# Kernel tuning notes

Measured on AMD Instinct MI355X. Metric: run time of the kernel, lower is better.

Reference implementation:

```python
import jax, jax.numpy as jnp
import numpy as np

DIM = 1024
HEADS = 16
DIM_HEAD = 64
SCALE = DIM_HEAD ** -0.5
LN_EPS = 1e-5


def layer_norm(x, g, b):
    mu = jnp.mean(x, axis=-1, keepdims=True)
    var = jnp.mean(jnp.square(x - mu), axis=-1, keepdims=True)
    return (x - mu) * jax.lax.rsqrt(var + LN_EPS) * g + b


def setup_inputs() -> dict:
    key = jax.random.key(0)
    ks = jax.random.split(key, 8)
    w_std = DIM ** -0.5  # keep GEMM outputs O(1)
    return {
        "query": jax.random.normal(ks[0], (4, 512, DIM), jnp.float32),
        "kv": jax.random.normal(ks[1], (4, 2048, DIM), jnp.float32),
        "ln_q_g": jnp.ones((DIM,), jnp.float32),
        "ln_q_b": jnp.zeros((DIM,), jnp.float32),
        "ln_kv_g": jnp.ones((DIM,), jnp.float32),
        "ln_kv_b": jnp.zeros((DIM,), jnp.float32),
        "Wq": jax.random.normal(ks[2], (DIM, DIM), jnp.float32) * w_std,
        "bq": jnp.zeros((DIM,), jnp.float32),
        "Wk": jax.random.normal(ks[3], (DIM, DIM), jnp.float32) * w_std,
        "bk": jnp.zeros((DIM,), jnp.float32),
        "Wv": jax.random.normal(ks[4], (DIM, DIM), jnp.float32) * w_std,
        "bv": jnp.zeros((DIM,), jnp.float32),
        "Wo": jax.random.normal(ks[5], (DIM, DIM), jnp.float32) * w_std,
        "bo": jnp.zeros((DIM,), jnp.float32),
    }


def reference(query, kv, ln_q_g, ln_q_b, ln_kv_g, ln_kv_b,
              Wq, bq, Wk, bk, Wv, bv, Wo, bo):
    kv_n = layer_norm(kv, ln_kv_g, ln_kv_b)            # (b, n_kv, d)
    residual = query
    q_n = layer_norm(query, ln_q_g, ln_q_b)            # (b, n_q, d)

    q = q_n @ Wq + bq                                   # (b, n_q, inner)
    kv_input = jnp.concatenate((kv_n, q_n), axis=-2)    # (b, n_kv+n_q, d)
    k = kv_input @ Wk + bk
    v = kv_input @ Wv + bv

    def split_heads(t):
        b, n, _ = t.shape
        return t.reshape(b, n, HEADS, DIM_HEAD).transpose(0, 2, 1, 3)  # b h n dh

    q = split_heads(q) * SCALE
    k = split_heads(k)
    v = split_heads(v)

    sim = jnp.einsum('bhid,bhjd->bhij', q, k)           # (b, h, n_q, n_kv+n_q)
    sim = sim - jax.lax.stop_gradient(jnp.max(sim, axis=-1, keepdims=True))
    attn = jax.nn.softmax(sim, axis=-1)
    out = jnp.einsum('bhij,bhjd->bhid', attn, v)        # (b, h, n_q, dh)

    b, h, n, dh = out.shape
    out = out.transpose(0, 2, 1, 3).reshape(b, n, h * dh)
    return out @ Wo + bo + residual
```

## Files before the change

kernel.cpp:

```cpp
#include <hip/hip_runtime.h>
#include <hip/hip_bf16.h>

#define B_    4
#define NQ    512
#define NKV   2048
#define NT    2560
#define DIM_  1024
#define HEADS 16
#define DH    64
#define NSEQT 10240
#define SCALE_Q_L2E 0.18033688011112042f

typedef short bf16x8 __attribute__((ext_vector_type(8)));
typedef float f32x4  __attribute__((ext_vector_type(4)));
typedef __hip_bfloat16 bf16;

__device__ inline void gll16(const bf16* g, bf16* l) {
  __builtin_amdgcn_global_load_lds(
      (const __attribute__((address_space(1))) unsigned int*)g,
      (__attribute__((address_space(3))) unsigned int*)l, 16, 0, 0);
}

__global__ __launch_bounds__(256) void ln_kernel(
    const float* __restrict__ query, const float* __restrict__ kv,
    const float* __restrict__ gq, const float* __restrict__ bq,
    const float* __restrict__ gkv, const float* __restrict__ bkv,
    bf16* __restrict__ X)
{
  int row = blockIdx.x;
  int b = row / NT, r = row % NT;
  const float *src, *g, *bb;
  if (r < NKV) { src = kv    + ((size_t)b*NKV + r)*DIM_;        g = gkv; bb = bkv; }
  else         { src = query + ((size_t)b*NQ + (r-NKV))*DIM_;   g = gq;  bb = bq;  }
  int t = threadIdx.x;
  float4 v = ((const float4*)src)[t];
  float s  = v.x+v.y+v.z+v.w;
  float s2 = v.x*v.x+v.y*v.y+v.z*v.z+v.w*v.w;
  #pragma unroll
  for (int m=1;m<64;m<<=1){ s += __shfl_xor(s,m,64); s2 += __shfl_xor(s2,m,64); }
  __shared__ float sh[8];
  int wave=t>>6, lane=t&63;
  if(lane==0){ sh[wave]=s; sh[4+wave]=s2; }
  __syncthreads();
  s  = sh[0]+sh[1]+sh[2]+sh[3];
  s2 = sh[4]+sh[5]+sh[6]+sh[7];
  float mu = s*(1.0f/DIM_);
  float rs = rsqrtf(s2*(1.0f/DIM_) - mu*mu + 1e-5f);
  float4 gg = ((const float4*)g)[t];
  float4 b4 = ((const float4*)bb)[t];
  bf16* dst = X + (size_t)row*DIM_ + t*4;
  dst[0]=__float2bfloat16((v.x-mu)*rs*gg.x + b4.x);
  dst[1]=__float2bfloat16((v.y-mu)*rs*gg.y + b4.y);
  dst[2]=__float2bfloat16((v.z-mu)*rs*gg.z + b4.z);
  dst[3]=__float2bfloat16((v.w-mu)*rs*gg.w + b4.w);
}

__global__ __launch_bounds__(256) void trw4_kernel(
    const float* __restrict__ W0, const float* __restrict__ W1,
    const float* __restrict__ W2, const float* __restrict__ W3,
    bf16* __restrict__ T0, bf16* __restrict__ T1,
    bf16* __restrict__ T2, bf16* __restrict__ T3)
{
  const float* W; bf16* Wt;
  switch (blockIdx.z) {
    case 0: W=W0; Wt=T0; break;
    case 1: W=W1; Wt=T1; break;
    case 2: W=W2; Wt=T2; break;
    default: W=W3; Wt=T3; break;
  }
  __shared__ __align__(16) bf16 Ws[64*72];
  int t = threadIdx.x;
  int k0 = blockIdx.x*64, n0 = blockIdx.y*64;
  int kr = t>>2, nseg = (t&3)*16;
  const float4* s4 = (const float4*)(W + (size_t)(k0+kr)*DIM_ + n0 + nseg);
  union { uint4 u[2]; bf16 h[16]; } pk;
  #pragma unroll
  for (int j=0;j<4;j++){
    float4 v = s4[j];
    pk.h[j*4+0]=__float2bfloat16(v.x); pk.h[j*4+1]=__float2bfloat16(v.y);
    pk.h[j*4+2]=__float2bfloat16(v.z); pk.h[j*4+3]=__float2bfloat16(v.w);
  }
  *(uint4*)(Ws + kr*72 + nseg)     = pk.u[0];
  *(uint4*)(Ws + kr*72 + nseg + 8) = pk.u[1];
  __syncthreads();
  int n = t&63, kseg = t>>6;
  union { uint4 u[2]; bf16 h[16]; } o;
  #pragma unroll
  for (int k=0;k<16;k++) o.h[k] = Ws[(kseg*16+k)*72 + n];
  bf16* dst = Wt + (size_t)(n0+n)*DIM_ + k0 + kseg*16;
  *(uint4*)dst = o.u[0];
  *(uint4*)(dst+8) = o.u[1];
}

template<int MODE>
__global__ __launch_bounds__(256) void gemm128(
    const bf16* __restrict__ A, const bf16* __restrict__ Wt,
    const float* __restrict__ bias, const float* __restrict__ residual,
    void* __restrict__ outv, int rows_per_batch, int row_offset,
    int a_batch_stride_rows, int n_seq, float scale)
{
  __shared__ __align__(16) bf16 As[128*32];
  __shared__ __align__(16) bf16 Bs[128*32];
  const int t = threadIdx.x;
  const int m0 = blockIdx.x*128, n0 = blockIdx.y*128;
  const int r0 = t>>2, c8 = (t&3)*8;

  int gm0 = m0 + r0, gm1 = m0 + 64 + r0;
  int b0i = gm0 / rows_per_batch, b1i = gm1 / rows_per_batch;
  const bf16* a0 = A + ((size_t)b0i*a_batch_stride_rows + row_offset + (gm0 - b0i*rows_per_batch))*DIM_ + c8;
  const bf16* a1 = A + ((size_t)b1i*a_batch_stride_rows + row_offset + (gm1 - b1i*rows_per_batch))*DIM_ + c8;
  const bf16* wb0 = Wt + (size_t)(n0 + r0)*DIM_ + c8;
  const bf16* wb1 = Wt + (size_t)(n0 + 64 + r0)*DIM_ + c8;
  bf16* lA0 = As + t*8;  bf16* lA1 = As + 64*32 + t*8;
  bf16* lB0 = Bs + t*8;  bf16* lB1 = Bs + 64*32 + t*8;

  const int wave = t>>6, lane = t&63, qq = lane>>4, mr = lane&15;
  const int wm = (wave>>1)*64, wn = (wave&1)*64;

  f32x4 acc[4][4] = {};
  for (int k0 = 0; k0 < DIM_; k0 += 32) {
    gll16(a0 + k0, lA0);
    gll16(a1 + k0, lA1);
    gll16(wb0 + k0, lB0);
    gll16(wb1 + k0, lB1);
    __syncthreads();
    bf16x8 af[4], bfr[4];
    #pragma unroll
    for (int ms=0;ms<4;ms++) af[ms]  = *(const bf16x8*)(As + (wm+ms*16+mr)*32 + qq*8);
    #pragma unroll
    for (int ns=0;ns<4;ns++) bfr[ns] = *(const bf16x8*)(Bs + (wn+ns*16+mr)*32 + qq*8);
    #pragma unroll
    for (int ms=0;ms<4;ms++)
      #pragma unroll
      for (int ns=0;ns<4;ns++)
        acc[ms][ns] = __builtin_amdgcn_mfma_f32_16x16x32_bf16(af[ms], bfr[ns], acc[ms][ns], 0,0,0);
    __syncthreads();
  }

  if (MODE == 0) {
    float* out = (float*)outv;
    #pragma unroll
    for (int ms=0;ms<4;ms++) {
      int row = m0 + wm + ms*16 + qq*4;
      #pragma unroll
      for (int ns=0;ns<4;ns++) {
        int col = n0 + wn + ns*16 + mr;
        float bc = bias[col];
        #pragma unroll
        for (int r=0;r<4;r++) {
          size_t idx = (size_t)(row+r)*DIM_ + col;
          out[idx] = acc[ms][ns][r] + bc + residual[idx];
        }
      }
    }
  } else if (MODE == 1) {
    bf16* out = (bf16*)outv;
    #pragma unroll
    for (int ms=0;ms<4;ms++) {
      int gmb = m0 + wm + ms*16 + qq*4;
      size_t rowbase[4];
      #pragma unroll
      for (int r=0;r<4;r++) {
        int gm = gmb + r;
        int bb = gm / rows_per_batch;
        int n  = gm - bb*rows_per_batch;
        rowbase[r] = ((size_t)bb*HEADS*n_seq + n)*DH;
      }
      #pragma unroll
      for (int ns=0;ns<4;ns++) {
        int col = n0 + wn + ns*16 + mr;
        int hh = col>>6, dh = col&63;
        float bc = bias[col];
        size_t hoff = (size_t)hh*n_seq*DH + dh;
        #pragma unroll
        for (int r=0;r<4;r++)
          out[rowbase[r] + hoff] = __float2bfloat16((acc[ms][ns][r] + bc)*scale);
      }
    }
  } else {
    bf16* out = (bf16*)outv;
    #pragma unroll
    for (int ms=0;ms<4;ms++) {
      int ch = m0 + wm + ms*16 + qq*4;
      #pragma unroll
      for (int r=0;r<4;r++) {
        float bc = bias[ch+r];
        #pragma unroll
        for (int ns=0;ns<4;ns++) {
          int col = n0 + wn + ns*16 + mr;
          out[(size_t)(ch+r)*NSEQT + col] = __float2bfloat16(acc[ms][ns][r] + bc);
        }
      }
    }
  }
}

__global__ __launch_bounds__(256) void attn5_kernel(
    const bf16* __restrict__ Qh, const bf16* __restrict__ Kh,
    const bf16* __restrict__ VTg, bf16* __restrict__ Ctx)
{
  __shared__ __align__(16) bf16 KV[2][8192];
  __shared__ __align__(16) unsigned int Ps[4][576];

  const int t = threadIdx.x, wave = t>>6, lane = t&63;
  const int qq = lane>>4, mr = lane&15;
  const int blk = blockIdx.x;
  const int bh = (blk&7)*8 + (blk>>6);
  const int q0 = ((blk>>3)&7)*64;
  const int b = bh>>4, h = bh&15;

  const int sl = t>>2, sc = t&3;
  const int skey = ((sl&15)<<2) | (sl>>4);
  const bf16* Kb  = Kh + (size_t)bh*NT*DH + (size_t)skey*DH + sc*8;
  const bf16* VbT = VTg + ((size_t)(h*DH) + sl)*NSEQT + (size_t)b*NT + sc*8;

  const bf16* Qb = Qh + ((size_t)bh*NQ + q0 + wave*16 + mr)*DH;
  bf16x8 qf0 = *(const bf16x8*)(Qb + qq*8);
  bf16x8 qf1 = *(const bf16x8*)(Qb + 32 + qq*8);

  f32x4 o[4] = {};
  float l[4] = {};
  unsigned int* Pw = &Ps[wave][0];

  {
    bf16* bp = &KV[0][0];
    gll16(Kb,            bp + t*8);
    gll16(Kb + 32,       bp + 2048 + t*8);
    gll16(VbT,           bp + 4096 + t*8);
    gll16(VbT + 32,      bp + 6144 + t*8);
  }

  for (int it = 0; it < NT/64; it++) {
    __syncthreads();
    if (it + 1 < NT/64) {
      int kt = (it+1)*64;
      bf16* bp = &KV[(it+1)&1][0];
      gll16(Kb  + (size_t)kt*DH, bp + t*8);
      gll16(Kb  + (size_t)kt*DH + 32, bp + 2048 + t*8);
      gll16(VbT + kt,      bp + 4096 + t*8);
      gll16(VbT + kt + 32, bp + 6144 + t*8);
    }
    const bf16* cbuf = &KV[it&1][0];

    bf16x8 kl[4], kh_[4];
    #pragma unroll
    for (int g=0; g<4; g++){
      kl[g]  = *(const bf16x8*)(cbuf + ((g*16+mr)*32 + qq*8));
      kh_[g] = *(const bf16x8*)(cbuf + 2048 + ((g*16+mr)*32 + qq*8));
    }
    f32x4 s[4];
    #pragma unroll
    for (int g=0; g<4; g++){
      f32x4 z = {};
      z = __builtin_amdgcn_mfma_f32_16x16x32_bf16(qf0, kl[g],  z, 0,0,0);
      z = __builtin_amdgcn_mfma_f32_16x16x32_bf16(qf1, kh_[g], z, 0,0,0);
      s[g] = z;
    }
    bf16x8 vl[4], vh[4];
    #pragma unroll
    for (int n2=0; n2<4; n2++){
      vl[n2] = *(const bf16x8*)(cbuf + 4096 + ((n2*16+mr)*32 + qq*8));
      vh[n2] = *(const bf16x8*)(cbuf + 6144 + ((n2*16+mr)*32 + qq*8));
    }
    #pragma unroll
    for (int r=0; r<4; r++){
      float e0 = __builtin_amdgcn_exp2f(s[0][r]);
      float e1 = __builtin_amdgcn_exp2f(s[1][r]);
      float e2 = __builtin_amdgcn_exp2f(s[2][r]);
      float e3 = __builtin_amdgcn_exp2f(s[3][r]);
      l[r] += (e0+e1)+(e2+e3);
      unsigned a0 = __float_as_uint(e0) + 0x8000u;
      unsigned a1 = __float_as_uint(e1) + 0x8000u;
      unsigned a2 = __float_as_uint(e2) + 0x8000u;
      unsigned a3 = __float_as_uint(e3) + 0x8000u;
      uint2 w;
      w.x = __builtin_amdgcn_perm(a1, a0, 0x07060302u);
      w.y = __builtin_amdgcn_perm(a3, a2, 0x07060302u);
      *(uint2*)(Pw + (qq*4+r)*36 + mr*2) = w;
    }
    asm volatile("s_waitcnt lgkmcnt(0)" ::: "memory");
    bf16x8 plo = *(const bf16x8*)(Pw + mr*36 + qq*4);
    bf16x8 phi = *(const bf16x8*)(Pw + mr*36 + qq*4 + 16);
    #pragma unroll
    for (int n2=0; n2<4; n2++){
      o[n2] = __builtin_amdgcn_mfma_f32_16x16x32_bf16(plo, vl[n2], o[n2], 0,0,0);
      o[n2] = __builtin_amdgcn_mfma_f32_16x16x32_bf16(phi, vh[n2], o[n2], 0,0,0);
    }
  }

  float rl[4];
  #pragma unroll
  for (int r=0; r<4; r++){
    float v = l[r];
    #pragma unroll
    for (int m=1;m<16;m<<=1) v += __shfl_xor(v, m, 16);
    rl[r] = 1.0f / v;
  }

  __syncthreads();
  float* OfW = (float*)(&KV[0][0]) + wave*1088;
  #pragma unroll
  for (int n2=0; n2<4; n2++)
    #pragma unroll
    for (int r=0; r<4; r++)
      OfW[(qq*4+r)*68 + n2*16 + mr] = o[n2][r]*rl[r];
  asm volatile("s_waitcnt lgkmcnt(0)" ::: "memory");
  {
    int row = lane>>2, seg = (lane&3)*16;
    union { uint4 u[2]; bf16 hh[16]; } pkv;
    #pragma unroll
    for (int j=0;j<16;j++) pkv.hh[j] = __float2bfloat16(OfW[row*68 + seg + j]);
    bf16* dst = Ctx + ((size_t)b*NQ + q0 + wave*16 + row)*DIM_ + h*DH + seg;
    *(uint4*)dst = pkv.u[0];
    *(uint4*)(dst+8) = pkv.u[1];
  }
}

extern "C" void kernel_launch(void* const* d_in, const int* in_sizes, int n_in,
                              void* d_out, int out_size, void* d_ws, size_t ws_size,
                              hipStream_t stream)
{
  const float* query  = (const float*)d_in[0];
  const float* kv     = (const float*)d_in[1];
  const float* ln_q_g = (const float*)d_in[2];
  const float* ln_q_b = (const float*)d_in[3];
  const float* ln_kv_g= (const float*)d_in[4];
  const float* ln_kv_b= (const float*)d_in[5];
  const float* Wq = (const float*)d_in[6];
  const float* bq = (const float*)d_in[7];
  const float* Wk = (const float*)d_in[8];
  const float* bk = (const float*)d_in[9];
  const float* Wv = (const float*)d_in[10];
  const float* bv = (const float*)d_in[11];
  const float* Wo = (const float*)d_in[12];
  const float* bo = (const float*)d_in[13];
  float* out = (float*)d_out;

  char* ws = (char*)d_ws;
  size_t off = 0;
  auto take = [&](size_t bytes)->char* {
    char* p = ws + off; off += (bytes + 255) & ~(size_t)255; return p;
  };
  bf16* X    = (bf16*)take((size_t)B_*NT*DIM_*2);
  bf16* Qhb  = (bf16*)take((size_t)B_*NQ*DIM_*2);
  bf16* Khb  = (bf16*)take((size_t)B_*NT*DIM_*2);
  bf16* VTg  = (bf16*)take((size_t)DIM_*NSEQT*2);
  bf16* Ctx  = (bf16*)take((size_t)B_*NQ*DIM_*2);
  bf16* WtQ  = (bf16*)take((size_t)DIM_*DIM_*2);
  bf16* WtK  = (bf16*)take((size_t)DIM_*DIM_*2);
  bf16* WtV  = (bf16*)take((size_t)DIM_*DIM_*2);
  bf16* WtO  = (bf16*)take((size_t)DIM_*DIM_*2);

  trw4_kernel<<<dim3(16,16,4), 256, 0, stream>>>(Wq, Wk, Wv, Wo,
                                                 WtQ, WtK, WtV, WtO);

  ln_kernel<<<B_*NT, 256, 0, stream>>>(query, kv, ln_q_g, ln_q_b,
                                       ln_kv_g, ln_kv_b, X);

  gemm128<1><<<dim3(16,8), 256, 0, stream>>>(X, WtQ, bq, nullptr, Qhb,
                                             NQ, NKV, NT, NQ, SCALE_Q_L2E);
  gemm128<1><<<dim3(80,8), 256, 0, stream>>>(X, WtK, bk, nullptr, Khb,
                                             NT, 0, NT, NT, 1.0f);
  gemm128<2><<<dim3(8,80), 256, 0, stream>>>(WtV, X, bv, nullptr, VTg,
                                             DIM_, 0, DIM_, NSEQT, 1.0f);

  attn5_kernel<<<512, 256, 0, stream>>>(Qhb, Khb, VTg, Ctx);

  gemm128<0><<<dim3(16,8), 256, 0, stream>>>(Ctx, WtO, bo, query, out,
                                             NQ, 0, NQ, NQ, 1.0f);
}
```

Before: 269.0 us.

## Widen GEMM K-step to 64 with XOR-swizzled LDS and staged vectorized epilogue

```diff
diff --git a/kernel.cpp b/kernel.cpp
--- a/kernel.cpp
+++ b/kernel.cpp
@@ -99,98 +99,112 @@
     void* __restrict__ outv, int rows_per_batch, int row_offset,
     int a_batch_stride_rows, int n_seq, float scale)
 {
-  __shared__ __align__(16) bf16 As[128*32];
-  __shared__ __align__(16) bf16 Bs[128*32];
+  __shared__ __align__(16) char smem[32768];
+  bf16* As = (bf16*)smem;
+  bf16* Bs = (bf16*)(smem + 16384);
+  float* Ts = (float*)smem;
+
   const int t = threadIdx.x;
   const int m0 = blockIdx.x*128, n0 = blockIdx.y*128;
-  const int r0 = t>>2, c8 = (t&3)*8;
-
-  int gm0 = m0 + r0, gm1 = m0 + 64 + r0;
-  int b0i = gm0 / rows_per_batch, b1i = gm1 / rows_per_batch;
-  const bf16* a0 = A + ((size_t)b0i*a_batch_stride_rows + row_offset + (gm0 - b0i*rows_per_batch))*DIM_ + c8;
-  const bf16* a1 = A + ((size_t)b1i*a_batch_stride_rows + row_offset + (gm1 - b1i*rows_per_batch))*DIM_ + c8;
-  const bf16* wb0 = Wt + (size_t)(n0 + r0)*DIM_ + c8;
-  const bf16* wb1 = Wt + (size_t)(n0 + 64 + r0)*DIM_ + c8;
-  bf16* lA0 = As + t*8;  bf16* lA1 = As + 64*32 + t*8;
-  bf16* lB0 = Bs + t*8;  bf16* lB1 = Bs + 64*32 + t*8;
+
+  const int srow = t>>3;
+  const int c = (t&7) ^ (srow&7);
+  const bf16* aptr[4];
+  const bf16* bptr[4];
+  #pragma unroll
+  for (int j=0;j<4;j++){
+    int r = j*32 + srow;
+    int gm = m0 + r;
+    int bb = gm / rows_per_batch;
+    aptr[j] = A + ((size_t)bb*a_batch_stride_rows + row_offset + (gm - bb*rows_per_batch))*(size_t)DIM_ + c*8;
+    bptr[j] = Wt + (size_t)(n0 + r)*DIM_ + c*8;
+  }
+  bf16* lA = As + t*8;
+  bf16* lB = Bs + t*8;
 
   const int wave = t>>6, lane = t&63, qq = lane>>4, mr = lane&15;
   const int wm = (wave>>1)*64, wn = (wave&1)*64;
+  const int sw = mr&7;
 
   f32x4 acc[4][4] = {};
-  for (int k0 = 0; k0 < DIM_; k0 += 32) {
-    gll16(a0 + k0, lA0);
-    gll16(a1 + k0, lA1);
-    gll16(wb0 + k0, lB0);
-    gll16(wb1 + k0, lB1);
-    __syncthreads();
-    bf16x8 af[4], bfr[4];
-    #pragma unroll
-    for (int ms=0;ms<4;ms++) af[ms]  = *(const bf16x8*)(As + (wm+ms*16+mr)*32 + qq*8);
-    #pragma unroll
-    for (int ns=0;ns<4;ns++) bfr[ns] = *(const bf16x8*)(Bs + (wn+ns*16+mr)*32 + qq*8);
-    #pragma unroll
-    for (int ms=0;ms<4;ms++)
-      #pragma unroll
-      for (int ns=0;ns<4;ns++)
-        acc[ms][ns] = __builtin_amdgcn_mfma_f32_16x16x32_bf16(af[ms], bfr[ns], acc[ms][ns], 0,0,0);
-    __syncthreads();
-  }
-
-  if (MODE == 0) {
-    float* out = (float*)outv;
-    #pragma unroll
-    for (int ms=0;ms<4;ms++) {
-      int row = m0 + wm + ms*16 + qq*4;
-      #pragma unroll
-      for (int ns=0;ns<4;ns++) {
-        int col = n0 + wn + ns*16 + mr;
-        float bc = bias[col];
+  for (int k0 = 0; k0 < DIM_; k0 += 64) {
+    #pragma unroll
+    for (int j=0;j<4;j++){
+      gll16(aptr[j] + k0, lA + j*2048);
+      gll16(bptr[j] + k0, lB + j*2048);
+    }
+    __syncthreads();
+    #pragma unroll
+    for (int ko=0; ko<2; ko++){
+      const int slot = ((ko*4 + qq) ^ sw) * 8;
+      bf16x8 af[4], bfr[4];
+      #pragma unroll
+      for (int ms=0;ms<4;ms++) af[ms]  = *(const bf16x8*)(As + (wm+ms*16+mr)*64 + slot);
+      #pragma unroll
+      for (int ns=0;ns<4;ns++) bfr[ns] = *(const bf16x8*)(Bs + (wn+ns*16+mr)*64 + slot);
+      #pragma unroll
+      for (int ms=0;ms<4;ms++)
         #pragma unroll
-        for (int r=0;r<4;r++) {
-          size_t idx = (size_t)(row+r)*DIM_ + col;
-          out[idx] = acc[ms][ns][r] + bc + residual[idx];
-        }
+        for (int ns=0;ns<4;ns++)
+          acc[ms][ns] = __builtin_amdgcn_mfma_f32_16x16x32_bf16(af[ms], bfr[ns], acc[ms][ns], 0,0,0);
+    }
+    __syncthreads();
+  }
+
+  const int lr = t>>3;
+  const int cs = (t&7)*16;
+  const int wlr = (wave>>1)*16 + qq*4;
+  #pragma unroll
+  for (int ms=0; ms<4; ms++){
+    __syncthreads();
+    #pragma unroll
+    for (int ns=0; ns<4; ns++){
+      int col = wn + ns*16 + mr;
+      #pragma unroll
+      for (int r=0;r<4;r++)
+        Ts[(wlr+r)*132 + col] = acc[ms][ns][r];
+    }
+    __syncthreads();
+    float v[16];
+    #pragma unroll
+    for (int j=0;j<4;j++){
+      float4 f = *(const float4*)(Ts + lr*132 + cs + j*4);
+      v[j*4+0]=f.x; v[j*4+1]=f.y; v[j*4+2]=f.z; v[j*4+3]=f.w;
+    }
+    int gr = m0 + (lr>>4)*64 + ms*16 + (lr&15);
+    int gc = n0 + cs;
+    if (MODE == 0) {
+      float* out = (float*)outv;
+      size_t base = (size_t)gr*DIM_ + gc;
+      #pragma unroll
+      for (int j=0;j<4;j++){
+        float4 bv = *(const float4*)(bias + gc + j*4);
+        float4 rv = *(const float4*)(residual + base + j*4);
+        float4 o4;
+        o4.x = v[j*4+0] + bv.x + rv.x;
+        o4.y = v[j*4+1] + bv.y + rv.y;
+        o4.z = v[j*4+2] + bv.z + rv.z;
+        o4.w = v[j*4+3] + bv.w + rv.w;
+        *(float4*)(out + base + j*4) = o4;
       }
-    }
-  } else if (MODE == 1) {
-    bf16* out = (bf16*)outv;
-    #pragma unroll
-    for (int ms=0;ms<4;ms++) {
-      int gmb = m0 + wm + ms*16 + qq*4;
-      size_t rowbase[4];
-      #pragma unroll
-      for (int r=0;r<4;r++) {
-        int gm = gmb + r;
-        int bb = gm / rows_per_batch;
-        int n  = gm - bb*rows_per_batch;
-        rowbase[r] = ((size_t)bb*HEADS*n_seq + n)*DH;
-      }
-      #pragma unroll
-      for (int ns=0;ns<4;ns++) {
-        int col = n0 + wn + ns*16 + mr;
-        int hh = col>>6, dh = col&63;
-        float bc = bias[col];
-        size_t hoff = (size_t)hh*n_seq*DH + dh;
-        #pragma unroll
-        for (int r=0;r<4;r++)
-          out[rowbase[r] + hoff] = __float2bfloat16((acc[ms][ns][r] + bc)*scale);
-      }
-    }
-  } else {
-    bf16* out = (bf16*)outv;
-    #pragma unroll
-    for (int ms=0;ms<4;ms++) {
-      int ch = m0 + wm + ms*16 + qq*4;
-      #pragma unroll
-      for (int r=0;r<4;r++) {
-        float bc = bias[ch+r];
-        #pragma unroll
-        for (int ns=0;ns<4;ns++) {
-          int col = n0 + wn + ns*16 + mr;
-          out[(size_t)(ch+r)*NSEQT + col] = __float2bfloat16(acc[ms][ns][r] + bc);
-        }
-      }
+    } else if (MODE == 1) {
+      int bb = gr / rows_per_batch;
+      int n  = gr - bb*rows_per_batch;
+      int hh = gc>>6, dh = gc&63;
+      bf16* out = (bf16*)outv + ((size_t)(bb*HEADS + hh)*n_seq + n)*DH + dh;
+      union { uint4 u[2]; bf16 h[16]; } pk;
+      #pragma unroll
+      for (int j=0;j<16;j++) pk.h[j] = __float2bfloat16((v[j] + bias[gc+j])*scale);
+      *(uint4*)out     = pk.u[0];
+      *(uint4*)(out+8) = pk.u[1];
+    } else {
+      float bc = bias[gr];
+      bf16* out = (bf16*)outv + (size_t)gr*NSEQT + gc;
+      union { uint4 u[2]; bf16 h[16]; } pk;
+      #pragma unroll
+      for (int j=0;j<16;j++) pk.h[j] = __float2bfloat16(v[j] + bc);
+      *(uint4*)out     = pk.u[0];
+      *(uint4*)(out+8) = pk.u[1];
     }
   }
 }
```

New measurement: 285.1 us. 1.06x slower.
